# Optimization experiments

Measured on AMD Instinct MI355X. Metric: run time of the kernel, lower is better.

Reference implementation:

```python
import jax, jax.numpy as jnp
import numpy as np

B, T, D = 2, 2048, 2048
H, HKV = 16, 16
SEM, GEO = 1024, 1024
DH = D // H          # 128, v head dim
DS = SEM // H        # 64, sem head dim
DG = GEO // H        # 64, geo head dim (== rope_dim)
ROPE_BASE = 10000.0


def _split_heads(x, n_heads, hd):
    b, t, _ = x.shape
    return x.reshape(b, t, n_heads, hd).transpose(0, 2, 1, 3)  # (B,H,T,hd)


def _rope(x, pos_offset):
    # x: (B,H,T,DG); rotate-half RoPE over the full geo head dim
    b, h, t, d = x.shape
    inv_freq = 1.0 / (ROPE_BASE ** (jnp.arange(0, d, 2, dtype=jnp.float32) / d))
    pos = jnp.arange(t, dtype=jnp.float32) + jnp.float32(pos_offset)
    ang = pos[:, None] * inv_freq[None, :]            # (T, d/2)
    cos, sin = jnp.cos(ang), jnp.sin(ang)             # (T, d/2)
    x1, x2 = x[..., : d // 2], x[..., d // 2 :]
    return jnp.concatenate([x1 * cos - x2 * sin, x2 * cos + x1 * sin], axis=-1)


def setup_inputs() -> dict:
    key = jax.random.key(0)
    ks = jax.random.split(key, 8)
    s = lambda fan_in: 1.0 / np.sqrt(fan_in)
    return {
        "x": jax.random.normal(ks[0], (B, T, D), dtype=jnp.float32),
        "Wq_sem": jax.random.normal(ks[1], (D, SEM), dtype=jnp.float32) * s(D),
        "Wk_sem": jax.random.normal(ks[2], (D, SEM), dtype=jnp.float32) * s(D),
        "Wq_geo": jax.random.normal(ks[3], (D, GEO), dtype=jnp.float32) * s(D),
        "Wk_geo": jax.random.normal(ks[4], (D, GEO), dtype=jnp.float32) * s(D),
        "Wv": jax.random.normal(ks[5], (D, D), dtype=jnp.float32) * s(D),
        "Wo": jax.random.normal(ks[6], (D, D), dtype=jnp.float32) * s(D),
        "gate_logit": jax.random.normal(ks[7], (H,), dtype=jnp.float32) * 0.1,
        "pos_offset": 0,
    }


def reference(x, Wq_sem, Wk_sem, Wq_geo, Wk_geo, Wv, Wo, gate_logit, pos_offset):
    qsh = _split_heads(x @ Wq_sem, H, DS)    # (B,H,T,DS)
    ksh = _split_heads(x @ Wk_sem, HKV, DS)
    qgh = _split_heads(x @ Wq_geo, H, DG)    # (B,H,T,DG)
    kgh = _split_heads(x @ Wk_geo, HKV, DG)
    vh = _split_heads(x @ Wv, HKV, DH)       # (B,H,T,DH)

    qgh = _rope(qgh, pos_offset)
    kgh = _rope(kgh, pos_offset)

    gate = jax.nn.sigmoid(gate_logit).reshape(1, H, 1, 1).astype(x.dtype)
    qsh = qsh * (2.0 * gate)
    qgh = qgh * (2.0 - 2.0 * gate)

    sem_scale = 1.0 / np.sqrt(float(DS))
    geo_scale = 1.0 / np.sqrt(float(DG))
    # decoupled logits: sem and geo contributions each with their own scale
    logits = (jnp.einsum("bhqd,bhkd->bhqk", qsh, ksh) * sem_scale
              + jnp.einsum("bhqd,bhkd->bhqk", qgh, kgh) * geo_scale)

    t = x.shape[1]
    causal = jnp.tril(jnp.ones((t, t), dtype=bool))
    logits = jnp.where(causal, logits, jnp.finfo(logits.dtype).min)
    attn = jax.nn.softmax(logits, axis=-1)

    out_h = jnp.einsum("bhqk,bhkd->bhqd", attn, vh)   # (B,H,T,DH)
    out = out_h.transpose(0, 2, 1, 3).reshape(x.shape[0], t, H * DH)
    return out @ Wo
```

## Files before the change

kernel.cpp:

```cpp
#include <hip/hip_runtime.h>
#include <hip/hip_bf16.h>
#include <math.h>

#define B_ 2
#define T_ 2048
#define D_ 2048
#define H_ 16
#define DH_ 128
#define SEM_ 1024
#define GEO_ 1024
#define NPROJ 6144

typedef unsigned short ushort_t;
typedef short bf16x8 __attribute__((ext_vector_type(8)));
typedef float f32x4 __attribute__((ext_vector_type(4)));
typedef unsigned short us4 __attribute__((ext_vector_type(4)));

static __device__ inline ushort_t f2b(float x) {
    __hip_bfloat16 h = __float2bfloat16(x);
    return *reinterpret_cast<ushort_t*>(&h);
}
static __device__ inline float b2f(ushort_t u) {
    union { unsigned int i; float f; } v; v.i = ((unsigned int)u) << 16; return v.f;
}
static __device__ inline void gload_lds16(const ushort_t* g, ushort_t* l) {
    __builtin_amdgcn_global_load_lds(
        (const __attribute__((address_space(1))) void*)g,
        (__attribute__((address_space(3))) void*)l, 16, 0, 0);
}

__global__ __launch_bounds__(256) void convert_x(
    const float* __restrict__ x, ushort_t* __restrict__ xh)
{
    size_t i = ((size_t)blockIdx.x * 256 + threadIdx.x) * 8;
    float4 a = *(const float4*)&x[i];
    float4 b = *(const float4*)&x[i + 4];
    bf16x8 o;
    o[0] = (short)f2b(a.x); o[1] = (short)f2b(a.y);
    o[2] = (short)f2b(a.z); o[3] = (short)f2b(a.w);
    o[4] = (short)f2b(b.x); o[5] = (short)f2b(b.y);
    o[6] = (short)f2b(b.z); o[7] = (short)f2b(b.w);
    *(bf16x8*)&xh[i] = o;
}

__global__ __launch_bounds__(256) void transpose_all(
    const float* __restrict__ W0, const float* __restrict__ W1,
    const float* __restrict__ W2, const float* __restrict__ W3,
    const float* __restrict__ W4, const float* __restrict__ W5,
    ushort_t* __restrict__ Wt_all, ushort_t* __restrict__ WoT)
{
    const int z = blockIdx.z;
    const float* W;
    ushort_t* dst;
    int N;
    switch (z) {
        case 0: W = W0; dst = Wt_all;                          N = 1024; break;
        case 1: W = W1; dst = Wt_all + (size_t)1024 * 2048;    N = 1024; break;
        case 2: W = W2; dst = Wt_all + (size_t)2048 * 2048;    N = 1024; break;
        case 3: W = W3; dst = Wt_all + (size_t)3072 * 2048;    N = 1024; break;
        case 4: W = W4; dst = Wt_all + (size_t)4096 * 2048;    N = 2048; break;
        default: W = W5; dst = WoT;                            N = 2048; break;
    }
    const int n0 = blockIdx.x * 32;
    if (n0 >= N) return;
    const int k0 = blockIdx.y * 32;

    __shared__ float tile[32][33];
    const int c = threadIdx.x & 31, r = threadIdx.x >> 5;
#pragma unroll
    for (int rr = 0; rr < 32; rr += 8)
        tile[r + rr][c] = W[(size_t)(k0 + r + rr) * N + n0 + c];
    __syncthreads();
#pragma unroll
    for (int rr = 0; rr < 32; rr += 8)
        dst[(size_t)(n0 + r + rr) * 2048 + k0 + c] = f2b(tile[c][r + rr]);
}

#define BARS()  { asm volatile("" ::: "memory"); __builtin_amdgcn_s_barrier(); asm volatile("" ::: "memory"); }
#define WL0()   asm volatile("s_waitcnt lgkmcnt(0)" ::: "memory")
#define WV6()   asm volatile("s_waitcnt vmcnt(6)" ::: "memory")

#define LDA8(par, iq, i4, kk) \
    (*(const bf16x8*)&smA[(par)*16384 + (iq)*8192 + aoff + (i4)*1024 + ((kk) ? ca1 : ca0)])
#define LDB8(par, jq, j1, kk) \
    (*(const bf16x8*)&smB[(par)*16384 + (jq)*8192 + boff + (j1)*2048 + ((kk) ? ca1 : ca0)])

#define READ_A(par, iq) \
    aF[0]=LDA8(par,iq,0,0); aF[1]=LDA8(par,iq,0,1); \
    aF[2]=LDA8(par,iq,1,0); aF[3]=LDA8(par,iq,1,1); \
    aF[4]=LDA8(par,iq,2,0); aF[5]=LDA8(par,iq,2,1); \
    aF[6]=LDA8(par,iq,3,0); aF[7]=LDA8(par,iq,3,1);

#define READ_B(par, jq) \
    bF[(jq)*4+0]=LDB8(par,jq,0,0); bF[(jq)*4+1]=LDB8(par,jq,0,1); \
    bF[(jq)*4+2]=LDB8(par,jq,1,0); bF[(jq)*4+3]=LDB8(par,jq,1,1);

#define STAGE_A(h, kt, par) do { \
    const ushort_t* _s = gAbase + (size_t)((h)*128) * 2048 + (kt)*64 + stgoff; \
    ushort_t* _d = smA + (par)*16384 + (h)*8192 + wid*512; \
    gload_lds16(_s, _d); \
    gload_lds16(_s + (size_t)64*2048, _d + 4096); \
} while(0)

#define STAGE_B(h, kt, par) do { \
    const ushort_t* _s = gBbase + (size_t)((h)*128) * 2048 + (kt)*64 + stgoff; \
    ushort_t* _d = smB + (par)*16384 + (h)*8192 + wid*512; \
    gload_lds16(_s, _d); \
    gload_lds16(_s + (size_t)64*2048, _d + 4096); \
} while(0)

#define MM16(iq, jq) do { \
    _Pragma("unroll") \
    for (int i4 = 0; i4 < 4; ++i4) { \
        acc[(iq)*4+i4][(jq)*2+0] = __builtin_amdgcn_mfma_f32_16x16x32_bf16(aF[i4*2+0], bF[(jq)*4+0], acc[(iq)*4+i4][(jq)*2+0], 0, 0, 0); \
        acc[(iq)*4+i4][(jq)*2+0] = __builtin_amdgcn_mfma_f32_16x16x32_bf16(aF[i4*2+1], bF[(jq)*4+1], acc[(iq)*4+i4][(jq)*2+0], 0, 0, 0); \
        acc[(iq)*4+i4][(jq)*2+1] = __builtin_amdgcn_mfma_f32_16x16x32_bf16(aF[i4*2+0], bF[(jq)*4+2], acc[(iq)*4+i4][(jq)*2+1], 0, 0, 0); \
        acc[(iq)*4+i4][(jq)*2+1] = __builtin_amdgcn_mfma_f32_16x16x32_bf16(aF[i4*2+1], bF[(jq)*4+3], acc[(iq)*4+i4][(jq)*2+1], 0, 0, 0); \
    } \
} while(0)

#define TILE_BODY(par, parn, kt1, kt2) \
    STAGE_A(1, kt1, parn); \
    BARS(); WL0(); \
    __builtin_amdgcn_s_setprio(1); MM16(0, 0); __builtin_amdgcn_s_setprio(0); \
    READ_B(par, 1); \
    BARS(); \
    STAGE_A(0, kt2, par); \
    BARS(); WL0(); \
    __builtin_amdgcn_s_setprio(1); MM16(0, 1); __builtin_amdgcn_s_setprio(0); \
    READ_A(par, 1); \
    BARS(); \
    STAGE_B(0, kt2, par); \
    BARS(); WL0(); \
    __builtin_amdgcn_s_setprio(1); MM16(1, 1); __builtin_amdgcn_s_setprio(0); \
    BARS(); \
    STAGE_B(1, kt2, par); WV6(); \
    BARS(); \
    __builtin_amdgcn_s_setprio(1); MM16(1, 0); __builtin_amdgcn_s_setprio(0); \
    READ_A(parn, 0); READ_B(parn, 0); \
    BARS();

__global__ __launch_bounds__(512, 2) void gemm_proj(
    const ushort_t* __restrict__ A, const ushort_t* __restrict__ Bt,
    const float* __restrict__ gate_logit, const int* __restrict__ pos_off,
    ushort_t* __restrict__ Qh, ushort_t* __restrict__ Kh,
    ushort_t* __restrict__ Vt)
{
    extern __shared__ __align__(16) ushort_t smdyn[];
    ushort_t* smA = smdyn;
    ushort_t* smB = smdyn + 32768;

    const int tid  = threadIdx.x;
    const int wid  = tid >> 6, lane = tid & 63;
    const int ln16 = lane & 15, g = lane >> 4;
    const int wm = wid & 1, wn = wid >> 1;
    const int m0 = blockIdx.y * 256, n0 = blockIdx.x * 256;

    const int srow = wid * 8 + (lane >> 3);
    const int scol = ((lane & 7) ^ (lane >> 3)) * 8;
    const size_t stgoff = (size_t)srow * 2048 + scol;
    const ushort_t* gAbase = A  + (size_t)m0 * 2048;
    const ushort_t* gBbase = Bt + (size_t)n0 * 2048;

    const int cg0 = ln16 & 7;
    const int ca0 = ((g + 0) ^ cg0) * 8;
    const int ca1 = ((g + 4) ^ cg0) * 8;
    const int aoff = wm * 4096 + ln16 * 64;
    const int boff = (wn >> 1) * 4096 + (wn & 1) * 1024 + ln16 * 64;

    f32x4 acc[8][4];
#pragma unroll
    for (int i = 0; i < 8; ++i)
#pragma unroll
        for (int j = 0; j < 4; ++j) acc[i][j] = (f32x4){0.f, 0.f, 0.f, 0.f};
    bf16x8 aF[8], bF[8];

    STAGE_A(0, 0, 0); STAGE_B(0, 0, 0); STAGE_B(1, 0, 0); STAGE_A(1, 0, 0);
    STAGE_A(0, 1, 1); STAGE_B(0, 1, 1); STAGE_B(1, 1, 1);
    WV6();
    BARS();
    READ_A(0, 0); READ_B(0, 0);

#pragma unroll 1
    for (int t = 0; t < 32; t += 2) {
        const int ka1 = t + 1;
        const int ka2 = (t + 2 < 32) ? t + 2 : 31;
        const int kb1 = ka2;
        const int kb2 = (t + 3 < 32) ? t + 3 : 31;
        TILE_BODY(0, 1, ka1, ka2);
        TILE_BODY(1, 0, kb1, kb2);
    }
    asm volatile("s_waitcnt vmcnt(0) lgkmcnt(0)" ::: "memory");

    const int region = n0 >> 10;
    const int rbase  = m0 + wm * 64 + g * 4;

    if (region <= 1) {
        ushort_t* dst = (region == 0) ? Qh : Kh;
        const int hb  = ((n0 & 1023) >> 6) + (wn >> 1);
        const int d64 = (wn & 1) * 16 + ln16;
        float sc0 = 1.0f, sc1 = 1.0f;
        if (region == 0) {
            sc0 = 0.25f / (1.0f + __expf(-gate_logit[hb]));
            sc1 = 0.25f / (1.0f + __expf(-gate_logit[hb + 2]));
        }
#pragma unroll
        for (int i = 0; i < 8; ++i)
#pragma unroll
            for (int r = 0; r < 4; ++r) {
                int row = rbase + (i >> 2) * 128 + (i & 3) * 16 + r;
                int t = row & (T_ - 1), bb = row >> 11;
                size_t b0 = ((size_t)(bb * H_ + hb)     * T_ + t) * 128;
                size_t b1 = ((size_t)(bb * H_ + hb + 2) * T_ + t) * 128;
                dst[b0 + d64]      = f2b(acc[i][0][r] * sc0);
                dst[b0 + d64 + 32] = f2b(acc[i][1][r] * sc0);
                dst[b1 + d64]      = f2b(acc[i][2][r] * sc1);
                dst[b1 + d64 + 32] = f2b(acc[i][3][r] * sc1);
            }
    } else if (region <= 3) {
        ushort_t* dst = (region == 2) ? Qh : Kh;
        const int hb = ((n0 & 1023) >> 6) + (wn >> 1);
        const int ip = (wn & 1) * 16 + ln16;
        const float invf = __expf(-0.28782313665087625f * (float)ip);
        const float po = (float)(*pos_off);
        float sc0 = 1.0f, sc1 = 1.0f;
        if (region == 2) {
            sc0 = 0.25f * (1.0f - 1.0f / (1.0f + __expf(-gate_logit[hb])));
            sc1 = 0.25f * (1.0f - 1.0f / (1.0f + __expf(-gate_logit[hb + 2])));
        }
#pragma unroll
        for (int i = 0; i < 8; ++i)
#pragma unroll
            for (int r = 0; r < 4; ++r) {
                int row = rbase + (i >> 2) * 128 + (i & 3) * 16 + r;
                int t = row & (T_ - 1), bb = row >> 11;
                float s, c;
                __sincosf(((float)t + po) * invf, &s, &c);
                size_t b0 = ((size_t)(bb * H_ + hb)     * T_ + t) * 128;
                size_t b1 = ((size_t)(bb * H_ + hb + 2) * T_ + t) * 128;
                float x1 = acc[i][0][r], x2 = acc[i][1][r];
                dst[b0 + 64 + ip] = f2b((x1 * c - x2 * s) * sc0);
                dst[b0 + 96 + ip] = f2b((x2 * c + x1 * s) * sc0);
                x1 = acc[i][2][r]; x2 = acc[i][3][r];
                dst[b1 + 64 + ip] = f2b((x1 * c - x2 * s) * sc1);
                dst[b1 + 96 + ip] = f2b((x2 * c + x1 * s) * sc1);
            }
    } else {
        const int hb = (n0 - 4096) >> 7;
        const int db = (wn >> 1) * 64 + (wn & 1) * 16 + ln16;
#pragma unroll
        for (int i = 0; i < 8; ++i) {
            int row0 = rbase + (i >> 2) * 128 + (i & 3) * 16;
            int t0 = row0 & (T_ - 1), bb = row0 >> 11;
#pragma unroll
            for (int j = 0; j < 4; ++j) {
                us4 v;
                v[0] = f2b(acc[i][j][0]); v[1] = f2b(acc[i][j][1]);
                v[2] = f2b(acc[i][j][2]); v[3] = f2b(acc[i][j][3]);
                int hh = hb + (j >> 1);
                int dd = db + (j & 1) * 32;
                *(us4*)&Vt[((size_t)(bb * H_ + hh) * DH_ + dd) * T_ + t0] = v;
            }
        }
    }
}

__global__ __launch_bounds__(256) void gemm_bt_f32(
    const ushort_t* __restrict__ A, const ushort_t* __restrict__ Bt,
    float* __restrict__ C, int M, int N, int K)
{
    __shared__ ushort_t As[128 * 32];
    __shared__ ushort_t Bs[128 * 32];

    const int tid  = threadIdx.x;
    const int wid  = tid >> 6, lane = tid & 63;
    const int ln16 = lane & 15, g = lane >> 4;
    const int wm = wid & 1, wn = wid >> 1;
    const int m0 = blockIdx.y * 128, n0 = blockIdx.x * 128;

    const int lrow = lane >> 2;
    const int lc8  = (lane & 3) * 8;
    const ushort_t* gA = A  + (size_t)(m0 + wid * 32 + lrow) * K + lc8;
    const ushort_t* gB = Bt + (size_t)(n0 + wid * 32 + lrow) * K + lc8;
    ushort_t* lA = As + wid * 1024;
    ushort_t* lB = Bs + wid * 1024;
    const size_t K16 = (size_t)16 * K;

    f32x4 acc[4][4];
#pragma unroll
    for (int i = 0; i < 4; ++i)
#pragma unroll
        for (int j = 0; j < 4; ++j) acc[i][j] = (f32x4){0.f, 0.f, 0.f, 0.f};

    for (int k0 = 0; k0 < K; k0 += 32) {
        __syncthreads();
        gload_lds16(gA,       lA);
        gload_lds16(gA + K16, lA + 512);
        gload_lds16(gB,       lB);
        gload_lds16(gB + K16, lB + 512);
        gA += 32; gB += 32;
        __syncthreads();

        bf16x8 af[4], bfr[4];
#pragma unroll
        for (int i = 0; i < 4; ++i)
            af[i] = *(const bf16x8*)&As[(wm * 64 + i * 16 + ln16) * 32 + g * 8];
#pragma unroll
        for (int j = 0; j < 4; ++j)
            bfr[j] = *(const bf16x8*)&Bs[(wn * 64 + j * 16 + ln16) * 32 + g * 8];
#pragma unroll
        for (int i = 0; i < 4; ++i)
#pragma unroll
            for (int j = 0; j < 4; ++j)
                acc[i][j] = __builtin_amdgcn_mfma_f32_16x16x32_bf16(
                    af[i], bfr[j], acc[i][j], 0, 0, 0);
    }

#pragma unroll
    for (int i = 0; i < 4; ++i)
#pragma unroll
        for (int j = 0; j < 4; ++j)
#pragma unroll
            for (int r = 0; r < 4; ++r) {
                int row = m0 + wm * 64 + i * 16 + g * 4 + r;
                int col = n0 + wn * 64 + j * 16 + ln16;
                C[(size_t)row * N + col] = acc[i][j][r];
            }
}

#define P_PITCH  40

#define FA_STAGE(kt, buf) do { \
    gload_lds16(Kbase + (size_t)((kt) + kr0) * 128 + kofs0, Ks + (buf)*4096 + wid * 512); \
    gload_lds16(Kbase + (size_t)((kt) + kr1) * 128 + kofs1, Ks + (buf)*4096 + 2048 + wid * 512); \
    gload_lds16(Vbase + (size_t)vd0 * T_ + (kt) + vofs0,    Vs + (buf)*4096 + wid * 512); \
    gload_lds16(Vbase + (size_t)vd1 * T_ + (kt) + vofs1,    Vs + (buf)*4096 + 2048 + wid * 512); \
} while(0)

__global__ __launch_bounds__(256) void flash_attn(
    const ushort_t* __restrict__ Qh,
    const ushort_t* __restrict__ Kh,
    const ushort_t* __restrict__ Vt,
    ushort_t* __restrict__ aoh)
{
    __shared__ ushort_t Ks[2 * 32 * 128];
    __shared__ ushort_t Vs[2 * 128 * 32];
    __shared__ ushort_t Pl[4 * 16 * P_PITCH];

    const int tid  = threadIdx.x;
    const int wid  = tid >> 6, lane = tid & 63;
    const int ln16 = lane & 15, g = lane >> 4;

    const int lin = blockIdx.x + (blockIdx.y << 4) + (blockIdx.z << 8);
    const int h = lin & 15;
    const int b = (lin >> 4) & 1;
    const int p = lin >> 5;
    const int bh = b * H_ + h;

    const ushort_t* Kbase = Kh + (size_t)bh * T_ * 128;
    const ushort_t* Vbase = Vt + (size_t)bh * 128 * T_;
    ushort_t* Pw = Pl + wid * 16 * P_PITCH;

    const int sk0 = tid,      sk1 = 256 + tid;
    const int kr0 = sk0 >> 4, kc0 = sk0 & 15;
    const int kr1 = sk1 >> 4, kc1 = sk1 & 15;
    const int vd0 = sk0 >> 2, vg0 = sk0 & 3;
    const int vd1 = sk1 >> 2, vg1 = sk1 & 3;
    const int kofs0 = (kc0 ^ (kr0 & 15)) * 8, kofs1 = (kc1 ^ (kr1 & 15)) * 8;
    const int vofs0 = (vg0 ^ ((vd0 + (vd0 >> 2)) & 3)) * 8;
    const int vofs1 = (vg1 ^ ((vd1 + (vd1 >> 2)) & 3)) * 8;

    bf16x8 bones;
    {
        short o = (ln16 == 0) ? (short)0x3F80 : (short)0;
#pragma unroll
        for (int j = 0; j < 8; ++j) bones[j] = o;
    }

#pragma unroll 1
    for (int ti = 0; ti < 2; ++ti) {
        const int qt = ti ? (31 - p) : p;
        const int q0 = qt * 64;
        const int qw = q0 + wid * 16;

        bf16x8 aq[4];
        {
            const ushort_t* qrow = Qh + ((size_t)bh * T_ + qw + ln16) * 128;
#pragma unroll
            for (int c2 = 0; c2 < 4; ++c2)
                aq[c2] = *(const bf16x8*)(qrow + c2 * 32 + g * 8);
        }

        f32x4 acc[8];
#pragma unroll
        for (int i = 0; i < 8; ++i) acc[i] = (f32x4){0.f, 0.f, 0.f, 0.f};
        f32x4 acc_l = (f32x4){0.f, 0.f, 0.f, 0.f};

        const int nkb  = q0 / 32 + 2;
        const int qmax = qw + 15;

        FA_STAGE(0, 0);
        asm volatile("s_waitcnt vmcnt(0)" ::: "memory");
        BARS();

#pragma unroll 1
        for (int kb = 0; kb < nkb; ++kb) {
            const int kt = kb * 32;
            if (kb + 1 < nkb) FA_STAGE(kt + 32, (kb + 1) & 1);

            if (kt <= qmax) {
                const int kbuf = (kb & 1) * 4096;

                f32x4 s0 = (f32x4){0.f, 0.f, 0.f, 0.f};
                f32x4 s1 = (f32x4){0.f, 0.f, 0.f, 0.f};
                __builtin_amdgcn_s_setprio(1);
#pragma unroll
                for (int c2 = 0; c2 < 4; ++c2) {
                    int jk = c2 * 4 + g;
                    bf16x8 bk0 = *(const bf16x8*)&Ks[kbuf + (ln16 * 16 + (jk ^ ln16)) * 8];
                    bf16x8 bk1 = *(const bf16x8*)&Ks[kbuf + (256 + ln16 * 16 + (jk ^ ln16)) * 8];
                    s0 = __builtin_amdgcn_mfma_f32_16x16x32_bf16(aq[c2], bk0, s0, 0, 0, 0);
                    s1 = __builtin_amdgcn_mfma_f32_16x16x32_bf16(aq[c2], bk1, s1, 0, 0, 0);
                }
                __builtin_amdgcn_s_setprio(0);

                const bool diag = (kt + 31 > qw);
#pragma unroll
                for (int r2 = 0; r2 < 4; ++r2) {
                    float e0 = __expf(s0[r2] - 12.0f);
                    float e1 = __expf(s1[r2] - 12.0f);
                    if (diag) {
                        int qr = qw + g * 4 + r2;
                        e0 = (kt + ln16      > qr) ? 0.0f : e0;
                        e1 = (kt + 16 + ln16 > qr) ? 0.0f : e1;
                    }
                    int prow = g * 4 + r2;
                    Pw[prow * P_PITCH + ln16]      = f2b(e0);
                    Pw[prow * P_PITCH + 16 + ln16] = f2b(e1);
                }
                __asm__ volatile("s_waitcnt lgkmcnt(0)" ::: "memory");
                bf16x8 ap = *(const bf16x8*)&Pw[ln16 * P_PITCH + g * 8];

                __builtin_amdgcn_s_setprio(1);
#pragma unroll
                for (int cdv = 0; cdv < 8; ++cdv) {
                    int d = cdv * 16 + ln16;
                    bf16x8 bv = *(const bf16x8*)
                        &Vs[kbuf + ((d << 2) + (g ^ ((d + (d >> 2)) & 3))) * 8];
                    acc[cdv] = __builtin_amdgcn_mfma_f32_16x16x32_bf16(ap, bv, acc[cdv], 0, 0, 0);
                }
                acc_l = __builtin_amdgcn_mfma_f32_16x16x32_bf16(ap, bones, acc_l, 0, 0, 0);
                __builtin_amdgcn_s_setprio(0);
            }

            asm volatile("s_waitcnt vmcnt(0)" ::: "memory");
            BARS();
        }

        float invl[4];
#pragma unroll
        for (int r2 = 0; r2 < 4; ++r2)
            invl[r2] = 1.0f / __shfl(acc_l[r2], lane & 48);
#pragma unroll
        for (int cdv = 0; cdv < 8; ++cdv)
#pragma unroll
            for (int r2 = 0; r2 < 4; ++r2) {
                int qr = qw + g * 4 + r2;
                aoh[((size_t)b * T_ + qr) * D_ + h * DH_ + cdv * 16 + ln16] =
                    f2b(acc[cdv][r2] * invl[r2]);
            }
    }
}

extern "C" void kernel_launch(void* const* d_in, const int* in_sizes, int n_in,
                              void* d_out, int out_size, void* d_ws, size_t ws_size,
                              hipStream_t stream)
{
    const float* x       = (const float*)d_in[0];
    const float* Wq_sem  = (const float*)d_in[1];
    const float* Wk_sem  = (const float*)d_in[2];
    const float* Wq_geo  = (const float*)d_in[3];
    const float* Wk_geo  = (const float*)d_in[4];
    const float* Wv      = (const float*)d_in[5];
    const float* Wo      = (const float*)d_in[6];
    const float* gate    = (const float*)d_in[7];
    const int*   pos_off = (const int*)d_in[8];
    float* out = (float*)d_out;

    const int M = B_ * T_;
    char* ws = (char*)d_ws;
    ushort_t* xh     = (ushort_t*)(ws);
    ushort_t* aoh    = xh;
    ushort_t* Wt_all = (ushort_t*)(ws + (size_t)16 * 1048576);
    ushort_t* WoT    = (ushort_t*)(ws + (size_t)40 * 1048576);
    ushort_t* Qh     = (ushort_t*)(ws + (size_t)48 * 1048576);
    ushort_t* Kh     = (ushort_t*)(ws + (size_t)64 * 1048576);
    ushort_t* Vt     = (ushort_t*)(ws + (size_t)80 * 1048576);

    dim3 blk(256);

    convert_x<<<(M * D_) / (256 * 8), blk, 0, stream>>>(x, xh);
    transpose_all<<<dim3(64, 64, 6), blk, 0, stream>>>(
        Wq_sem, Wk_sem, Wq_geo, Wk_geo, Wv, Wo, Wt_all, WoT);

    hipFuncSetAttribute((const void*)gemm_proj,
                        hipFuncAttributeMaxDynamicSharedMemorySize, 131072);
    gemm_proj<<<dim3(NPROJ / 256, M / 256), dim3(512), 131072, stream>>>(
        xh, Wt_all, gate, pos_off, Qh, Kh, Vt);

    flash_attn<<<dim3(16, H_, B_), blk, 0, stream>>>(Qh, Kh, Vt, aoh);

    gemm_bt_f32<<<dim3(D_ / 128, M / 128), blk, 0, stream>>>(
        aoh, WoT, out, M, D_, D_);
}
```

Before: 391.1 us.

## Double-buffer output GEMM and attention K/V loads, widen weight transpose tiles

The output-projection GEMM moves from a single-buffered LDS tile with two syncthreads per step to a two-stage double buffer. Loads for step k+2 are issued after compute, with vmcnt-based waits and setprio around the MFMAs. The flash-attention loop gets the same two-deep prefetch: both stages are issued up front and the wait is relaxed from vmcnt(0) to vmcnt(4). The weight transpose kernel switches to 64x64 tiles with float2 loads and paired bf16 stores, and its grid shrinks to match. Together these aim to hide global-load latency and cut transpose memory traffic, at the cost of doubled LDS use and hand-tuned waitcnt logic that must be exactly right.

```diff
diff --git a/kernel.cpp b/kernel.cpp
--- a/kernel.cpp
+++ b/kernel.cpp
@@ -15,6 +15,7 @@
 typedef short bf16x8 __attribute__((ext_vector_type(8)));
 typedef float f32x4 __attribute__((ext_vector_type(4)));
 typedef unsigned short us4 __attribute__((ext_vector_type(4)));
+typedef unsigned short us2 __attribute__((ext_vector_type(2)));
 
 static __device__ inline ushort_t f2b(float x) {
     __hip_bfloat16 h = __float2bfloat16(x);
@@ -28,6 +29,12 @@
         (const __attribute__((address_space(1))) void*)g,
         (__attribute__((address_space(3))) void*)l, 16, 0, 0);
 }
+
+#define BARS()  { asm volatile("" ::: "memory"); __builtin_amdgcn_s_barrier(); asm volatile("" ::: "memory"); }
+#define WL0()   asm volatile("s_waitcnt lgkmcnt(0)" ::: "memory")
+#define WV6()   asm volatile("s_waitcnt vmcnt(6)" ::: "memory")
+#define WV4()   asm volatile("s_waitcnt vmcnt(4)" ::: "memory")
+#define WV0()   asm volatile("s_waitcnt vmcnt(0)" ::: "memory")
 
 __global__ __launch_bounds__(256) void convert_x(
     const float* __restrict__ x, ushort_t* __restrict__ xh)
@@ -61,24 +68,30 @@
         case 4: W = W4; dst = Wt_all + (size_t)4096 * 2048;    N = 2048; break;
         default: W = W5; dst = WoT;                            N = 2048; break;
     }
-    const int n0 = blockIdx.x * 32;
+    const int n0 = blockIdx.x * 64;
     if (n0 >= N) return;
-    const int k0 = blockIdx.y * 32;
-
-    __shared__ float tile[32][33];
-    const int c = threadIdx.x & 31, r = threadIdx.x >> 5;
-#pragma unroll
-    for (int rr = 0; rr < 32; rr += 8)
-        tile[r + rr][c] = W[(size_t)(k0 + r + rr) * N + n0 + c];
+    const int k0 = blockIdx.y * 64;
+
+    __shared__ float tile[64][66];
+    const int c2 = (threadIdx.x & 31) * 2;
+    const int r  = threadIdx.x >> 5;
+#pragma unroll
+    for (int rr = 0; rr < 64; rr += 8) {
+        float2 v = *(const float2*)&W[(size_t)(k0 + r + rr) * N + n0 + c2];
+        tile[r + rr][c2]     = v.x;
+        tile[r + rr][c2 + 1] = v.y;
+    }
     __syncthreads();
-#pragma unroll
-    for (int rr = 0; rr < 32; rr += 8)
-        dst[(size_t)(n0 + r + rr) * 2048 + k0 + c] = f2b(tile[c][r + rr]);
-}
-
-#define BARS()  { asm volatile("" ::: "memory"); __builtin_amdgcn_s_barrier(); asm volatile("" ::: "memory"); }
-#define WL0()   asm volatile("s_waitcnt lgkmcnt(0)" ::: "memory")
-#define WV6()   asm volatile("s_waitcnt vmcnt(6)" ::: "memory")
+    const int kc = (threadIdx.x & 31) * 2;
+#pragma unroll
+    for (int rr = 0; rr < 64; rr += 8) {
+        int nrow = r + rr;
+        us2 o;
+        o[0] = f2b(tile[kc][nrow]);
+        o[1] = f2b(tile[kc + 1][nrow]);
+        *(us2*)&dst[(size_t)(n0 + nrow) * 2048 + k0 + kc] = o;
+    }
+}
 
 #define LDA8(par, iq, i4, kk) \
     (*(const bf16x8*)&smA[(par)*16384 + (iq)*8192 + aoff + (i4)*1024 + ((kk) ? ca1 : ca0)])
@@ -265,12 +278,19 @@
     }
 }
 
+#define BT_STAGE(k, buf) do { \
+    gload_lds16(gA + (k),       As + (buf)*4096 + wid*1024); \
+    gload_lds16(gA + (k) + K16, As + (buf)*4096 + wid*1024 + 512); \
+    gload_lds16(gB + (k),       Bs + (buf)*4096 + wid*1024); \
+    gload_lds16(gB + (k) + K16, Bs + (buf)*4096 + wid*1024 + 512); \
+} while(0)
+
 __global__ __launch_bounds__(256) void gemm_bt_f32(
     const ushort_t* __restrict__ A, const ushort_t* __restrict__ Bt,
     float* __restrict__ C, int M, int N, int K)
 {
-    __shared__ ushort_t As[128 * 32];
-    __shared__ ushort_t Bs[128 * 32];
+    __shared__ ushort_t As[2 * 128 * 32];
+    __shared__ ushort_t Bs[2 * 128 * 32];
 
     const int tid  = threadIdx.x;
     const int wid  = tid >> 6, lane = tid & 63;
@@ -282,8 +302,6 @@
     const int lc8  = (lane & 3) * 8;
     const ushort_t* gA = A  + (size_t)(m0 + wid * 32 + lrow) * K + lc8;
     const ushort_t* gB = Bt + (size_t)(n0 + wid * 32 + lrow) * K + lc8;
-    ushort_t* lA = As + wid * 1024;
-    ushort_t* lB = Bs + wid * 1024;
     const size_t K16 = (size_t)16 * K;
 
     f32x4 acc[4][4];
@@ -292,28 +310,35 @@
 #pragma unroll
         for (int j = 0; j < 4; ++j) acc[i][j] = (f32x4){0.f, 0.f, 0.f, 0.f};
 
-    for (int k0 = 0; k0 < K; k0 += 32) {
-        __syncthreads();
-        gload_lds16(gA,       lA);
-        gload_lds16(gA + K16, lA + 512);
-        gload_lds16(gB,       lB);
-        gload_lds16(gB + K16, lB + 512);
-        gA += 32; gB += 32;
-        __syncthreads();
-
+    const int nk = K >> 5;
+    BT_STAGE(0, 0);
+    BT_STAGE(32, 1);
+
+#pragma unroll 1
+    for (int kb = 0; kb < nk; ++kb) {
+        if (kb + 1 < nk) { WV4(); } else { WV0(); }
+        BARS();
+
+        const int bufo = (kb & 1) * 4096;
         bf16x8 af[4], bfr[4];
 #pragma unroll
         for (int i = 0; i < 4; ++i)
-            af[i] = *(const bf16x8*)&As[(wm * 64 + i * 16 + ln16) * 32 + g * 8];
+            af[i] = *(const bf16x8*)&As[bufo + (wm * 64 + i * 16 + ln16) * 32 + g * 8];
 #pragma unroll
         for (int j = 0; j < 4; ++j)
-            bfr[j] = *(const bf16x8*)&Bs[(wn * 64 + j * 16 + ln16) * 32 + g * 8];
+            bfr[j] = *(const bf16x8*)&Bs[bufo + (wn * 64 + j * 16 + ln16) * 32 + g * 8];
+        __builtin_amdgcn_s_setprio(1);
 #pragma unroll
         for (int i = 0; i < 4; ++i)
 #pragma unroll
             for (int j = 0; j < 4; ++j)
                 acc[i][j] = __builtin_amdgcn_mfma_f32_16x16x32_bf16(
                     af[i], bfr[j], acc[i][j], 0, 0, 0);
+        __builtin_amdgcn_s_setprio(0);
+        WL0();
+        BARS();
+
+        if (kb + 2 < nk) BT_STAGE((size_t)(kb + 2) * 32, kb & 1);
     }
 
 #pragma unroll
@@ -400,13 +425,13 @@
         const int qmax = qw + 15;
 
         FA_STAGE(0, 0);
-        asm volatile("s_waitcnt vmcnt(0)" ::: "memory");
-        BARS();
+        FA_STAGE(32, 1);
 
 #pragma unroll 1
         for (int kb = 0; kb < nkb; ++kb) {
             const int kt = kb * 32;
-            if (kb + 1 < nkb) FA_STAGE(kt + 32, (kb + 1) & 1);
+            if (kb + 1 < nkb) { WV4(); } else { WV0(); }
+            BARS();
 
             if (kt <= qmax) {
                 const int kbuf = (kb & 1) * 4096;
@@ -451,10 +476,11 @@
                 }
                 acc_l = __builtin_amdgcn_mfma_f32_16x16x32_bf16(ap, bones, acc_l, 0, 0, 0);
                 __builtin_amdgcn_s_setprio(0);
+                WL0();
             }
 
-            asm volatile("s_waitcnt vmcnt(0)" ::: "memory");
             BARS();
+            if (kb + 2 < nkb) FA_STAGE(kt + 64, kb & 1);
         }
 
         float invl[4];
@@ -500,7 +526,7 @@
     dim3 blk(256);
 
     convert_x<<<(M * D_) / (256 * 8), blk, 0, stream>>>(x, xh);
-    transpose_all<<<dim3(64, 64, 6), blk, 0, stream>>>(
+    transpose_all<<<dim3(32, 32, 6), blk, 0, stream>>>(
         Wq_sem, Wk_sem, Wq_geo, Wk_geo, Wv, Wo, Wt_all, WoT);
 
     hipFuncSetAttribute((const void*)gemm_proj,
```

Measured after the change: 372.8 us. 4.7% less time.
